# Optimization experiments

Measured on AMD Instinct MI355X. Metric: run time of the kernel, lower is better.

## Reference

```python
import jax, jax.numpy as jnp
import numpy as np

B, D_IN, D_FEAT, N_EX, N_LAB = 4096, 512, 512, 20000, 100
P_FACTOR = 3.0
EPS = 1e-12  # torch F.normalize eps


def setup_inputs() -> dict:
    key = jax.random.key(0)
    k1, k2, k3, k4 = jax.random.split(key, 4)
    features = jax.random.normal(k1, (B, D_IN), dtype=jnp.float32)
    g_weight = jax.random.normal(k2, (D_FEAT, D_IN), dtype=jnp.float32) * (1.0 / np.sqrt(D_IN))
    ex_features = jax.random.normal(k3, (N_EX, D_IN), dtype=jnp.float32)
    ex_classes = jax.random.uniform(k4, (N_EX, N_LAB), dtype=jnp.float32)
    class_reps = jnp.eye(N_LAB, dtype=jnp.float32)  # one_hot(arange(num_labels)) since class_dim is None
    return {"features": features, "g_weight": g_weight, "ex_features": ex_features,
            "ex_classes": ex_classes, "class_reps": class_reps}


def _l2_normalize(x):
    n = jnp.linalg.norm(x, axis=-1, keepdims=True)
    return x / jnp.maximum(n, EPS)


def _l1_normalize(x):
    n = jnp.sum(jnp.abs(x), axis=-1, keepdims=True)
    return x / jnp.maximum(n, EPS)


def reference(features, g_weight, ex_features, ex_classes, class_reps):
    # g projection (bias-free linear)
    f = features @ g_weight.T          # [B, D_FEAT]
    e = ex_features @ g_weight.T       # [N_EX, D_FEAT]
    # exemplar class representations
    ex_class_reps = _l1_normalize(ex_classes) @ class_reps  # [N_EX, N_LAB]
    # cosine similarity
    s = _l2_normalize(f) @ _l2_normalize(e).T  # [B, N_EX]
    # power-sign activation then L1 row-normalize
    a = jnp.sign(s) * jnp.abs(s) ** P_FACTOR
    a = _l1_normalize(a)
    echo = a @ ex_class_reps           # [B, N_LAB]
    return echo
```

## Files before the change

kernel.cpp:

```cpp
#include <hip/hip_runtime.h>

#define B_ROWS 4096
#define D      512
#define N_EX   20000
#define EXP2   20096
#define N_LAB  100
#define LABP2  128
#define NT2    157
#define SPLITS 16

typedef __attribute__((ext_vector_type(8)))  short short8v;
typedef __attribute__((ext_vector_type(4)))  short short4v;
typedef __attribute__((ext_vector_type(4)))  float f32x4;
typedef __attribute__((ext_vector_type(16))) float f32x16;
typedef __attribute__((ext_vector_type(2)))  int   int2v;
typedef unsigned short u16;

__device__ __forceinline__ u16 f2bf(float x) {
    unsigned u = __builtin_bit_cast(unsigned, x);
    u = u + 0x7FFFu + ((u >> 16) & 1u);
    return (u16)(u >> 16);
}
__device__ __forceinline__ float bf2f(u16 h) {
    unsigned u = ((unsigned)h) << 16;
    return __builtin_bit_cast(float, u);
}

__device__ __forceinline__ float wave_reduce_sum(float v) {
    #pragma unroll
    for (int off = 32; off > 0; off >>= 1) v += __shfl_down(v, off, 64);
    return v;
}

__device__ __forceinline__ void gload16(const void* g, void* l) {
    __builtin_amdgcn_global_load_lds((const __attribute__((address_space(1))) void*)g,
                                     (__attribute__((address_space(3))) void*)l, 16, 0, 0);
}

__device__ __forceinline__ unsigned pk_bf16(float a, float b) {
    unsigned r;
    asm("v_cvt_pk_bf16_f32 %0, %1, %2" : "=v"(r) : "v"(a), "v"(b));
    return r;
}

__device__ __forceinline__ void swap_halves(unsigned &a, unsigned &b) {
#if __has_builtin(__builtin_amdgcn_permlane32_swap)
    int2v r = __builtin_amdgcn_permlane32_swap((int)a, (int)b, false, false);
    a = (unsigned)r[0]; b = (unsigned)r[1];
#else
    unsigned sa = (unsigned)__shfl_xor((int)a, 32, 64);
    unsigned sb = (unsigned)__shfl_xor((int)b, 32, 64);
    if (threadIdx.x & 32) a = sb; else b = sa;
#endif
}

#define MFMA16(a, b, c) __builtin_amdgcn_mfma_f32_16x16x32_bf16((a), (b), (c), 0, 0, 0)
#define MFMA32(a, b, c) __builtin_amdgcn_mfma_f32_32x32x16_bf16((a), (b), (c), 0, 0, 0)

__global__ __launch_bounds__(256)
void splitH_k(const float* __restrict__ src, u16* __restrict__ dst,
              int src_rows, int dst_rows) {
    int i8 = blockIdx.x * 256 + threadIdx.x;
    if (i8 >= dst_rows * 64) return;
    int row = i8 >> 6;
    int e = (i8 & 63) * 8;
    short8v h = {0,0,0,0,0,0,0,0};
    if (row < src_rows) {
        const float* p = &src[(size_t)row * D + e];
        float4 a = *(const float4*)p, b = *(const float4*)(p + 4);
        float v[8] = {a.x,a.y,a.z,a.w,b.x,b.y,b.z,b.w};
        #pragma unroll
        for (int j = 0; j < 8; ++j) h[j] = (short)f2bf(v[j]);
    }
    *(short8v*)&dst[(size_t)row * D + e] = h;
}

__global__ __launch_bounds__(512, 4)
void gemm128_k(const u16* __restrict__ A, const u16* __restrict__ B,
               u16* __restrict__ C) {
    __shared__ u16 BUF[2][128][128];
    const int tid = threadIdx.x;
    const int l = tid & 63, w = tid >> 6;
    const int wa = w >> 2, wb = w & 3;
    const int l31 = l & 31, l5 = l >> 5;
    const int m0 = blockIdx.x * 128, n0 = blockIdx.y * 128;
    const int qrow_in = l >> 4;
    const int gs = l & 15;

    f32x16 sacc[2] = {};

    auto STAGE = [&](int nx, int kc_) {
        const int kofs = kc_ * 64;
        #pragma unroll
        for (int i = 0; i < 4; ++i) {
            const int q = w * 4 + i;
            const int r = q * 4 + qrow_in;
            const int g = gs ^ (r & 15);
            const u16* src = (g < 8)
                ? &A[(size_t)(m0 + r) * D + kofs + g * 8]
                : &B[(size_t)(n0 + r) * D + kofs + (g - 8) * 8];
            gload16(src, (u16*)&BUF[nx][0][0] + q * 512);
        }
    };

    STAGE(0, 0);
    __syncthreads();
    int cur = 0;
    for (int kc = 0; kc < 8; ++kc) {
        if (kc < 7) STAGE(cur ^ 1, kc + 1);
        const u16* base = &BUF[cur][0][0];
        #pragma unroll
        for (int ks = 0; ks < 4; ++ks) {
            const int gk = ks * 2 + l5;
            short8v aX[2], bW;
            #pragma unroll
            for (int ei = 0; ei < 2; ++ei) {
                int r = wa * 64 + ei * 32 + l31;
                aX[ei] = *(const short8v*)(base + r * 128 + (gk ^ (r & 15)) * 8);
            }
            {
                int r = wb * 32 + l31;
                bW = *(const short8v*)(base + r * 128 + ((gk | 8) ^ (r & 15)) * 8);
            }
            sacc[0] = MFMA32(aX[0], bW, sacc[0]);
            sacc[1] = MFMA32(aX[1], bW, sacc[1]);
        }
        __syncthreads();
        cur ^= 1;
    }
    #pragma unroll
    for (int ei = 0; ei < 2; ++ei)
        #pragma unroll
        for (int r = 0; r < 16; ++r) {
            int row = m0 + wa * 64 + ei * 32 + (r & 3) + 8 * (r >> 2) + 4 * l5;
            int col = n0 + wb * 32 + l31;
            C[(size_t)row * D + col] = f2bf(sacc[ei][r]);
        }
}

__global__ __launch_bounds__(256, 2)
void proj_k(const float* __restrict__ X, const float* __restrict__ W,
            u16* __restrict__ Chi, int M) {
    __shared__ u16 AH[64][72], AL[64][72], BH[64][72];
    const int tid = threadIdx.x;
    const int lane = tid & 63, wave = tid >> 6;
    const int wm = wave >> 1, wn = wave & 1;
    const int l15 = lane & 15, l4 = lane >> 4;
    const int m0 = blockIdx.x * 64, n0 = blockIdx.y * 64;
    f32x4 acc[2][2] = {};
    for (int kc = 0; kc < 8; ++kc) {
        __syncthreads();
        #pragma unroll
        for (int s = 0; s < 2; ++s) {
            int ix = tid + s * 256;
            int r = ix >> 3, c = ix & 7;
            float va[8] = {0.f,0.f,0.f,0.f,0.f,0.f,0.f,0.f};
            if (m0 + r < M) {
                const float* p = &X[(size_t)(m0 + r) * D + kc * 64 + c * 8];
                float4 t0 = *(const float4*)p, t1 = *(const float4*)(p + 4);
                va[0]=t0.x; va[1]=t0.y; va[2]=t0.z; va[3]=t0.w;
                va[4]=t1.x; va[5]=t1.y; va[6]=t1.z; va[7]=t1.w;
            }
            short8v h, l;
            #pragma unroll
            for (int j = 0; j < 8; ++j) {
                u16 hh = f2bf(va[j]); h[j] = (short)hh; l[j] = (short)f2bf(va[j] - bf2f(hh));
            }
            *(short8v*)&AH[r][c*8] = h; *(short8v*)&AL[r][c*8] = l;
            const float* q = &W[(size_t)(n0 + r) * D + kc * 64 + c * 8];
            float4 s0 = *(const float4*)q, s1 = *(const float4*)(q + 4);
            float vb[8] = {s0.x,s0.y,s0.z,s0.w,s1.x,s1.y,s1.z,s1.w};
            #pragma unroll
            for (int j = 0; j < 8; ++j) h[j] = (short)f2bf(vb[j]);
            *(short8v*)&BH[r][c*8] = h;
        }
        __syncthreads();
        #pragma unroll
        for (int ks = 0; ks < 2; ++ks) {
            const int ko = ks * 32 + l4 * 8;
            short8v ah0 = *(const short8v*)&AH[wm*32      + l15][ko];
            short8v ah1 = *(const short8v*)&AH[wm*32 + 16 + l15][ko];
            short8v al0 = *(const short8v*)&AL[wm*32      + l15][ko];
            short8v al1 = *(const short8v*)&AL[wm*32 + 16 + l15][ko];
            short8v bh0 = *(const short8v*)&BH[wn*32      + l15][ko];
            short8v bh1 = *(const short8v*)&BH[wn*32 + 16 + l15][ko];
            acc[0][0] = MFMA16(ah0, bh0, acc[0][0]); acc[0][0] = MFMA16(al0, bh0, acc[0][0]);
            acc[0][1] = MFMA16(ah0, bh1, acc[0][1]); acc[0][1] = MFMA16(al0, bh1, acc[0][1]);
            acc[1][0] = MFMA16(ah1, bh0, acc[1][0]); acc[1][0] = MFMA16(al1, bh0, acc[1][0]);
            acc[1][1] = MFMA16(ah1, bh1, acc[1][1]); acc[1][1] = MFMA16(al1, bh1, acc[1][1]);
        }
    }
    #pragma unroll
    for (int mi = 0; mi < 2; ++mi)
      #pragma unroll
      for (int ni = 0; ni < 2; ++ni)
        #pragma unroll
        for (int r = 0; r < 4; ++r) {
            int row = m0 + wm*32 + mi*16 + l4*4 + r;
            int col = n0 + wn*32 + ni*16 + l15;
            Chi[(size_t)row * D + col] = f2bf(acc[mi][ni][r]);
        }
}

__global__ __launch_bounds__(128)
void l2norm_k(u16* __restrict__ hi) {
    const int row = blockIdx.x, tid = threadIdx.x;
    const size_t base = (size_t)row * D + tid * 4;
    short4v hv = *(short4v*)&hi[base];
    float v[4]; float ss = 0.f;
    #pragma unroll
    for (int j = 0; j < 4; ++j) { v[j] = bf2f((u16)hv[j]); ss += v[j] * v[j]; }
    ss = wave_reduce_sum(ss);
    __shared__ float red[2];
    if ((tid & 63) == 0) red[tid >> 6] = ss;
    __syncthreads();
    float inv = 1.0f / fmaxf(sqrtf(red[0] + red[1]), 1e-12f);
    short4v ho;
    #pragma unroll
    for (int j = 0; j < 4; ++j) ho[j] = (short)f2bf(v[j] * inv);
    *(short4v*)&hi[base] = ho;
}

__global__ __launch_bounds__(256)
void ecrT_k(const float* __restrict__ exc, const float* __restrict__ creps,
            u16* __restrict__ th) {
    __shared__ float CRT[N_LAB][101];
    __shared__ float EX[128][N_LAB];
    __shared__ float INV[128];
    __shared__ u16 OUT[LABP2][128];
    const int tid = threadIdx.x;
    const int e0 = blockIdx.x * 128;
    for (int i = tid; i < N_LAB * N_LAB; i += 256) {
        int c = i / N_LAB, lab = i % N_LAB;
        CRT[lab][c] = creps[i];
    }
    for (int i = tid; i < 128 * N_LAB; i += 256) {
        int el = i / N_LAB, c = i % N_LAB;
        int e = e0 + el;
        EX[el][c] = (e < N_EX) ? exc[(size_t)e * N_LAB + c] : 0.f;
    }
    __syncthreads();
    if (tid < 128) {
        float s = 0.f;
        for (int c = 0; c < N_LAB; ++c) s += fabsf(EX[tid][c]);
        INV[tid] = 1.0f / fmaxf(s, 1e-12f);
    }
    __syncthreads();
    const int lab = tid & 127;
    for (int el = tid >> 7; el < 128; el += 2) {
        float acc = 0.f;
        if (lab < N_LAB) {
            #pragma unroll 4
            for (int c = 0; c < N_LAB; ++c) acc += EX[el][c] * CRT[lab][c];
            acc *= INV[el];
        }
        OUT[lab][el] = f2bf(acc);
    }
    __syncthreads();
    for (int i = tid; i < LABP2 * 16; i += 256) {
        int lb = i >> 4, ch = i & 15;
        *(short8v*)&th[(size_t)lb * EXP2 + e0 + ch * 8] = *(const short8v*)&OUT[lb][ch * 8];
    }
}

__global__ __launch_bounds__(512, 4)
void fused_k(const u16* __restrict__ fnh, const u16* __restrict__ enh,
             const u16* __restrict__ ecth,
             float* __restrict__ nump, float* __restrict__ denp2) {
    __shared__ u16 BUF[2][128][128];
    const int tid = threadIdx.x;
    const int l = tid & 63, w = tid >> 6;
    const int we = w >> 2, wq = w & 3;
    const int l31 = l & 31, l5 = l >> 5;
    const int m0 = blockIdx.x * 128;
    const int split = blockIdx.y;
    const int qrow_in = l >> 4;
    const int gs = l & 15;

    union FragU { short8v s; unsigned u[4]; };

    f32x16 num_acc[4] = {};
    float den_th = 0.f;

    auto STAGE_AB = [&](int nx, int t_, int kc_) {
        const int e0_ = t_ * 128, kofs = kc_ * 64;
        #pragma unroll
        for (int i = 0; i < 4; ++i) {
            const int q = w * 4 + i;
            const int r = q * 4 + qrow_in;
            const int g = gs ^ (r & 15);
            const u16* src = (g < 8)
                ? &enh[(size_t)(e0_ + r) * D + kofs + g * 8]
                : &fnh[(size_t)(m0 + r) * D + kofs + (g - 8) * 8];
            gload16(src, (u16*)&BUF[nx][0][0] + q * 512);
        }
    };
    auto STAGE_WT = [&](int nx, int t_) {
        const int e0_ = t_ * 128;
        #pragma unroll
        for (int i = 0; i < 4; ++i) {
            const int q = w * 4 + i;
            const int lab = q * 4 + qrow_in;
            const int g = gs ^ (lab & 15);
            gload16(&ecth[(size_t)lab * EXP2 + e0_ + g * 8],
                    (u16*)&BUF[nx][0][0] + q * 512);
        }
    };

    STAGE_AB(0, split, 0);
    __syncthreads();
    int cur = 0;

    for (int t = split; t < NT2; t += SPLITS) {
        f32x16 sacc[2] = {};
        for (int kc = 0; kc < 8; ++kc) {
            if (kc < 7) STAGE_AB(cur ^ 1, t, kc + 1);
            else        STAGE_WT(cur ^ 1, t);
            const u16* base = &BUF[cur][0][0];
            #pragma unroll
            for (int ks = 0; ks < 4; ++ks) {
                const int gk = ks * 2 + l5;
                short8v aE[2], bF;
                #pragma unroll
                for (int ei = 0; ei < 2; ++ei) {
                    int r = we * 64 + ei * 32 + l31;
                    aE[ei] = *(const short8v*)(base + r * 128 + (gk ^ (r & 15)) * 8);
                }
                {
                    int r = wq * 32 + l31;
                    bF = *(const short8v*)(base + r * 128 + ((gk | 8) ^ (r & 15)) * 8);
                }
                sacc[0] = MFMA32(aE[0], bF, sacc[0]);
                sacc[1] = MFMA32(aE[1], bF, sacc[1]);
            }
            __syncthreads();
            cur ^= 1;
        }
        const int tn = t + SPLITS;
        if (tn < NT2) STAGE_AB(cur ^ 1, tn, 0);
        const u16* wbase = &BUF[cur][0][0];
        #pragma unroll
        for (int ei = 0; ei < 2; ++ei) {
            float a3[16];
            #pragma unroll
            for (int r = 0; r < 16; ++r) {
                float sv = sacc[ei][r];
                float c3 = sv * sv * sv;
                a3[r] = c3;
                den_th += fabsf(c3);
            }
            FragU fr[2];
            #pragma unroll
            for (int c = 0; c < 2; ++c) {
                unsigned p01 = pk_bf16(a3[c*8+0], a3[c*8+1]);
                unsigned p23 = pk_bf16(a3[c*8+2], a3[c*8+3]);
                unsigned p45 = pk_bf16(a3[c*8+4], a3[c*8+5]);
                unsigned p67 = pk_bf16(a3[c*8+6], a3[c*8+7]);
                swap_halves(p01, p45);
                swap_halves(p23, p67);
                fr[c].u[0] = p01; fr[c].u[1] = p23; fr[c].u[2] = p45; fr[c].u[3] = p67;
            }
            #pragma unroll
            for (int c = 0; c < 2; ++c) {
                const int gw = (we * 4 + ei * 2 + c) * 2 + l5;
                #pragma unroll
                for (int lt = 0; lt < 4; ++lt) {
                    int row = lt * 32 + l31;
                    short8v wf = *(const short8v*)(wbase + row * 128 + (gw ^ (row & 15)) * 8);
                    num_acc[lt] = MFMA32(fr[c].s, wf, num_acc[lt]);
                }
            }
        }
        __syncthreads();
        cur ^= 1;
    }

    {
        float v = den_th;
        v += __shfl_xor(v, 32, 64);
        if (l5 == 0)
            denp2[((size_t)split * 2 + we) * B_ROWS + m0 + wq * 32 + l31] = v;
    }

    float* SMf = (float*)&BUF[0][0][0];
    __syncthreads();
    #pragma unroll
    for (int half = 0; half < 2; ++half) {
        if (we == 1 && (wq >> 1) == half) {
            #pragma unroll
            for (int lt = 0; lt < 4; ++lt)
                #pragma unroll
                for (int r = 0; r < 16; ++r) {
                    int rowf = (r & 3) + 8 * (r >> 2) + 4 * l5;
                    SMf[((wq & 1) * 32 + rowf) * 128 + lt * 32 + l31] = num_acc[lt][r];
                }
        }
        __syncthreads();
        if (we == 0 && (wq >> 1) == half) {
            #pragma unroll
            for (int lt = 0; lt < 4; ++lt)
                #pragma unroll
                for (int r = 0; r < 16; ++r) {
                    int rowf = (r & 3) + 8 * (r >> 2) + 4 * l5;
                    float v = num_acc[lt][r] + SMf[((wq & 1) * 32 + rowf) * 128 + lt * 32 + l31];
                    int m = m0 + wq * 32 + rowf;
                    nump[((size_t)split * B_ROWS + m) * LABP2 + lt * 32 + l31] = v;
                }
        }
        __syncthreads();
    }
}

__global__ __launch_bounds__(128)
void finalize_k(const float* __restrict__ nump, const float* __restrict__ denp2,
                float* __restrict__ out) {
    const int row = blockIdx.x, tid = threadIdx.x;
    float den = 0.f;
    for (int s = 0; s < 2 * SPLITS; ++s)
        den += denp2[(size_t)s * B_ROWS + row];
    if (tid < N_LAB) {
        float acc = 0.f;
        for (int s = 0; s < SPLITS; ++s)
            acc += nump[((size_t)s * B_ROWS + row) * LABP2 + tid];
        out[(size_t)row * N_LAB + tid] = acc / fmaxf(den, 1e-12f);
    }
}

extern "C" void kernel_launch(void* const* d_in, const int* in_sizes, int n_in,
                              void* d_out, int out_size, void* d_ws, size_t ws_size,
                              hipStream_t stream) {
    (void)in_sizes; (void)n_in; (void)out_size; (void)ws_size;
    const float* features    = (const float*)d_in[0];
    const float* g_weight    = (const float*)d_in[1];
    const float* ex_features = (const float*)d_in[2];
    const float* ex_classes  = (const float*)d_in[3];
    const float* class_reps  = (const float*)d_in[4];
    float* out = (float*)d_out;

    size_t off = 0;
    auto alloc = [&](size_t bytes) {
        void* p = (char*)d_ws + off;
        off += (bytes + 255) & ~(size_t)255;
        return p;
    };
    u16* fnh = (u16*)alloc((size_t)B_ROWS * D * 2);
    u16* enh = (u16*)alloc((size_t)EXP2 * D * 2);
    u16* ecth = (u16*)alloc((size_t)LABP2 * EXP2 * 2);
    u16* wh  = (u16*)alloc((size_t)D * D * 2);
    float* nump  = (float*)alloc((size_t)SPLITS * B_ROWS * LABP2 * 4);
    float* denp2 = (float*)alloc((size_t)2 * SPLITS * B_ROWS * 4);
    u16* exh = (u16*)nump;

    splitH_k<<<(EXP2 * 64 + 255) / 256, 256, 0, stream>>>(ex_features, exh, N_EX, EXP2);
    splitH_k<<<(D * 64 + 255) / 256, 256, 0, stream>>>(g_weight, wh, D, D);
    gemm128_k<<<dim3(EXP2 / 128, 4), 512, 0, stream>>>(exh, wh, enh);
    proj_k<<<dim3(B_ROWS / 64, 8), 256, 0, stream>>>(features, g_weight, fnh, B_ROWS);
    l2norm_k<<<B_ROWS, 128, 0, stream>>>(fnh);
    l2norm_k<<<EXP2, 128, 0, stream>>>(enh);
    ecrT_k<<<NT2, 256, 0, stream>>>(ex_classes, class_reps, ecth);
    fused_k<<<dim3(B_ROWS / 128, SPLITS), 512, 0, stream>>>(fnh, enh, ecth, nump, denp2);
    finalize_k<<<B_ROWS, 128, 0, stream>>>(nump, denp2, out);
}
```

Baseline: 432.1 us.

## Merge feature/exemplar projections into one GEMM and widen fused tile to 256 rows

Features and exemplars are now converted to bf16 into one contiguous buffer and projected by a single gemm128_k launch, followed by one l2norm launch. This replaces the separate hi/lo-split proj_k kernel and the second l2norm launch, so the feature projection no longer carries the low-order correction term. fused_k now processes 256 query rows per block instead of 128, using separate LDS regions for exemplar, feature and class-weight tiles. Each exemplar tile and class-weight fragment is therefore reused across twice as many rows. In exchange the block needs 128 KB of LDS, the grid halves to 256 blocks, occupancy drops, and register pressure rises.

```diff
diff --git a/kernel.cpp b/kernel.cpp
--- a/kernel.cpp
+++ b/kernel.cpp
@@ -4,6 +4,7 @@
 #define D      512
 #define N_EX   20000
 #define EXP2   20096
+#define MPROJ  24192
 #define N_LAB  100
 #define LABP2  128
 #define NT2    157
@@ -11,7 +12,6 @@
 
 typedef __attribute__((ext_vector_type(8)))  short short8v;
 typedef __attribute__((ext_vector_type(4)))  short short4v;
-typedef __attribute__((ext_vector_type(4)))  float f32x4;
 typedef __attribute__((ext_vector_type(16))) float f32x16;
 typedef __attribute__((ext_vector_type(2)))  int   int2v;
 typedef unsigned short u16;
@@ -54,7 +54,6 @@
 #endif
 }
 
-#define MFMA16(a, b, c) __builtin_amdgcn_mfma_f32_16x16x32_bf16((a), (b), (c), 0, 0, 0)
 #define MFMA32(a, b, c) __builtin_amdgcn_mfma_f32_32x32x16_bf16((a), (b), (c), 0, 0, 0)
 
 __global__ __launch_bounds__(256)
@@ -138,70 +137,6 @@
         }
 }
 
-__global__ __launch_bounds__(256, 2)
-void proj_k(const float* __restrict__ X, const float* __restrict__ W,
-            u16* __restrict__ Chi, int M) {
-    __shared__ u16 AH[64][72], AL[64][72], BH[64][72];
-    const int tid = threadIdx.x;
-    const int lane = tid & 63, wave = tid >> 6;
-    const int wm = wave >> 1, wn = wave & 1;
-    const int l15 = lane & 15, l4 = lane >> 4;
-    const int m0 = blockIdx.x * 64, n0 = blockIdx.y * 64;
-    f32x4 acc[2][2] = {};
-    for (int kc = 0; kc < 8; ++kc) {
-        __syncthreads();
-        #pragma unroll
-        for (int s = 0; s < 2; ++s) {
-            int ix = tid + s * 256;
-            int r = ix >> 3, c = ix & 7;
-            float va[8] = {0.f,0.f,0.f,0.f,0.f,0.f,0.f,0.f};
-            if (m0 + r < M) {
-                const float* p = &X[(size_t)(m0 + r) * D + kc * 64 + c * 8];
-                float4 t0 = *(const float4*)p, t1 = *(const float4*)(p + 4);
-                va[0]=t0.x; va[1]=t0.y; va[2]=t0.z; va[3]=t0.w;
-                va[4]=t1.x; va[5]=t1.y; va[6]=t1.z; va[7]=t1.w;
-            }
-            short8v h, l;
-            #pragma unroll
-            for (int j = 0; j < 8; ++j) {
-                u16 hh = f2bf(va[j]); h[j] = (short)hh; l[j] = (short)f2bf(va[j] - bf2f(hh));
-            }
-            *(short8v*)&AH[r][c*8] = h; *(short8v*)&AL[r][c*8] = l;
-            const float* q = &W[(size_t)(n0 + r) * D + kc * 64 + c * 8];
-            float4 s0 = *(const float4*)q, s1 = *(const float4*)(q + 4);
-            float vb[8] = {s0.x,s0.y,s0.z,s0.w,s1.x,s1.y,s1.z,s1.w};
-            #pragma unroll
-            for (int j = 0; j < 8; ++j) h[j] = (short)f2bf(vb[j]);
-            *(short8v*)&BH[r][c*8] = h;
-        }
-        __syncthreads();
-        #pragma unroll
-        for (int ks = 0; ks < 2; ++ks) {
-            const int ko = ks * 32 + l4 * 8;
-            short8v ah0 = *(const short8v*)&AH[wm*32      + l15][ko];
-            short8v ah1 = *(const short8v*)&AH[wm*32 + 16 + l15][ko];
-            short8v al0 = *(const short8v*)&AL[wm*32      + l15][ko];
-            short8v al1 = *(const short8v*)&AL[wm*32 + 16 + l15][ko];
-            short8v bh0 = *(const short8v*)&BH[wn*32      + l15][ko];
-            short8v bh1 = *(const short8v*)&BH[wn*32 + 16 + l15][ko];
-            acc[0][0] = MFMA16(ah0, bh0, acc[0][0]); acc[0][0] = MFMA16(al0, bh0, acc[0][0]);
-            acc[0][1] = MFMA16(ah0, bh1, acc[0][1]); acc[0][1] = MFMA16(al0, bh1, acc[0][1]);
-            acc[1][0] = MFMA16(ah1, bh0, acc[1][0]); acc[1][0] = MFMA16(al1, bh0, acc[1][0]);
-            acc[1][1] = MFMA16(ah1, bh1, acc[1][1]); acc[1][1] = MFMA16(al1, bh1, acc[1][1]);
-        }
-    }
-    #pragma unroll
-    for (int mi = 0; mi < 2; ++mi)
-      #pragma unroll
-      for (int ni = 0; ni < 2; ++ni)
-        #pragma unroll
-        for (int r = 0; r < 4; ++r) {
-            int row = m0 + wm*32 + mi*16 + l4*4 + r;
-            int col = n0 + wn*32 + ni*16 + l15;
-            Chi[(size_t)row * D + col] = f2bf(acc[mi][ni][r]);
-        }
-}
-
 __global__ __launch_bounds__(128)
 void l2norm_k(u16* __restrict__ hi) {
     const int row = blockIdx.x, tid = threadIdx.x;
@@ -263,47 +198,52 @@
     }
 }
 
-__global__ __launch_bounds__(512, 4)
+__global__ __launch_bounds__(512, 2)
 void fused_k(const u16* __restrict__ fnh, const u16* __restrict__ enh,
              const u16* __restrict__ ecth,
              float* __restrict__ nump, float* __restrict__ denp2) {
-    __shared__ u16 BUF[2][128][128];
+    __shared__ u16 SMEM[65536];
+    u16* ENR = SMEM;
+    u16* FNR = SMEM + 16384;
+    u16* WTB = SMEM + 49152;
+
     const int tid = threadIdx.x;
     const int l = tid & 63, w = tid >> 6;
     const int we = w >> 2, wq = w & 3;
     const int l31 = l & 31, l5 = l >> 5;
-    const int m0 = blockIdx.x * 128;
+    const int m0 = blockIdx.x * 256;
     const int split = blockIdx.y;
-    const int qrow_in = l >> 4;
-    const int gs = l & 15;
 
     union FragU { short8v s; unsigned u[4]; };
 
-    f32x16 num_acc[4] = {};
-    float den_th = 0.f;
+    f32x16 num_acc[2][4] = {};
+    float den_th[2] = {0.f, 0.f};
 
     auto STAGE_AB = [&](int nx, int t_, int kc_) {
         const int e0_ = t_ * 128, kofs = kc_ * 64;
         #pragma unroll
+        for (int i = 0; i < 2; ++i) {
+            const int ge = w * 128 + i * 64 + l;
+            const int row = ge >> 3, g = ge & 7;
+            gload16(&enh[(size_t)(e0_ + row) * D + kofs + ((g ^ (row & 7)) * 8)],
+                    ENR + nx * 8192 + (w * 128 + i * 64) * 8);
+        }
+        #pragma unroll
         for (int i = 0; i < 4; ++i) {
-            const int q = w * 4 + i;
-            const int r = q * 4 + qrow_in;
-            const int g = gs ^ (r & 15);
-            const u16* src = (g < 8)
-                ? &enh[(size_t)(e0_ + r) * D + kofs + g * 8]
-                : &fnh[(size_t)(m0 + r) * D + kofs + (g - 8) * 8];
-            gload16(src, (u16*)&BUF[nx][0][0] + q * 512);
+            const int gf = w * 256 + i * 64 + l;
+            const int row = gf >> 3, g = gf & 7;
+            gload16(&fnh[(size_t)(m0 + row) * D + kofs + ((g ^ (row & 7)) * 8)],
+                    FNR + nx * 16384 + (w * 256 + i * 64) * 8);
         }
     };
-    auto STAGE_WT = [&](int nx, int t_) {
+    auto STAGE_WT = [&](int t_) {
         const int e0_ = t_ * 128;
         #pragma unroll
         for (int i = 0; i < 4; ++i) {
-            const int q = w * 4 + i;
-            const int lab = q * 4 + qrow_in;
-            const int g = gs ^ (lab & 15);
-            gload16(&ecth[(size_t)lab * EXP2 + e0_ + g * 8],
-                    (u16*)&BUF[nx][0][0] + q * 512);
+            const int gwt = w * 256 + i * 64 + l;
+            const int lab = gwt >> 4, g = gwt & 15;
+            gload16(&ecth[(size_t)lab * EXP2 + e0_ + ((g ^ (lab & 15)) * 8)],
+                    WTB + (w * 256 + i * 64) * 8);
         }
     };
 
@@ -312,53 +252,61 @@
     int cur = 0;
 
     for (int t = split; t < NT2; t += SPLITS) {
-        f32x16 sacc[2] = {};
+        f32x16 sacc[2][2] = {};
         for (int kc = 0; kc < 8; ++kc) {
             if (kc < 7) STAGE_AB(cur ^ 1, t, kc + 1);
-            else        STAGE_WT(cur ^ 1, t);
-            const u16* base = &BUF[cur][0][0];
+            else        STAGE_WT(t);
+            const u16* eb = ENR + cur * 8192;
+            const u16* fb = FNR + cur * 16384;
             #pragma unroll
             for (int ks = 0; ks < 4; ++ks) {
                 const int gk = ks * 2 + l5;
-                short8v aE[2], bF;
+                short8v aE[2], bF[2];
                 #pragma unroll
                 for (int ei = 0; ei < 2; ++ei) {
                     int r = we * 64 + ei * 32 + l31;
-                    aE[ei] = *(const short8v*)(base + r * 128 + (gk ^ (r & 15)) * 8);
+                    aE[ei] = *(const short8v*)(eb + r * 64 + (gk ^ (r & 7)) * 8);
                 }
-                {
-                    int r = wq * 32 + l31;
-                    bF = *(const short8v*)(base + r * 128 + ((gk | 8) ^ (r & 15)) * 8);
+                #pragma unroll
+                for (int mi = 0; mi < 2; ++mi) {
+                    int r = wq * 64 + mi * 32 + l31;
+                    bF[mi] = *(const short8v*)(fb + r * 64 + (gk ^ (r & 7)) * 8);
                 }
-                sacc[0] = MFMA32(aE[0], bF, sacc[0]);
-                sacc[1] = MFMA32(aE[1], bF, sacc[1]);
+                #pragma unroll
+                for (int ei = 0; ei < 2; ++ei)
+                    #pragma unroll
+                    for (int mi = 0; mi < 2; ++mi)
+                        sacc[ei][mi] = MFMA32(aE[ei], bF[mi], sacc[ei][mi]);
             }
             __syncthreads();
-            cur ^= 1;
+            if (kc < 7) cur ^= 1;
         }
         const int tn = t + SPLITS;
         if (tn < NT2) STAGE_AB(cur ^ 1, tn, 0);
-        const u16* wbase = &BUF[cur][0][0];
         #pragma unroll
         for (int ei = 0; ei < 2; ++ei) {
-            float a3[16];
-            #pragma unroll
-            for (int r = 0; r < 16; ++r) {
-                float sv = sacc[ei][r];
-                float c3 = sv * sv * sv;
-                a3[r] = c3;
-                den_th += fabsf(c3);
-            }
-            FragU fr[2];
-            #pragma unroll
-            for (int c = 0; c < 2; ++c) {
-                unsigned p01 = pk_bf16(a3[c*8+0], a3[c*8+1]);
-                unsigned p23 = pk_bf16(a3[c*8+2], a3[c*8+3]);
-                unsigned p45 = pk_bf16(a3[c*8+4], a3[c*8+5]);
-                unsigned p67 = pk_bf16(a3[c*8+6], a3[c*8+7]);
-                swap_halves(p01, p45);
-                swap_halves(p23, p67);
-                fr[c].u[0] = p01; fr[c].u[1] = p23; fr[c].u[2] = p45; fr[c].u[3] = p67;
+            FragU fr[2][2];
+            #pragma unroll
+            for (int mi = 0; mi < 2; ++mi) {
+                float a3[16];
+                #pragma unroll
+                for (int r = 0; r < 16; ++r) {
+                    float sv = sacc[ei][mi][r];
+                    float c3 = sv * sv * sv;
+                    a3[r] = c3;
+                    den_th[mi] += fabsf(c3);
+                }
+                #pragma unroll
+                for (int c = 0; c < 2; ++c) {
+                    unsigned p01 = pk_bf16(a3[c*8+0], a3[c*8+1]);
+                    unsigned p23 = pk_bf16(a3[c*8+2], a3[c*8+3]);
+                    unsigned p45 = pk_bf16(a3[c*8+4], a3[c*8+5]);
+                    unsigned p67 = pk_bf16(a3[c*8+6], a3[c*8+7]);
+                    swap_halves(p01, p45);
+                    swap_halves(p23, p67);
+                    fr[mi][c].u[0] = p01; fr[mi][c].u[1] = p23;
+                    fr[mi][c].u[2] = p45; fr[mi][c].u[3] = p67;
+                }
             }
             #pragma unroll
             for (int c = 0; c < 2; ++c) {
@@ -366,8 +314,9 @@
                 #pragma unroll
                 for (int lt = 0; lt < 4; ++lt) {
                     int row = lt * 32 + l31;
-                    short8v wf = *(const short8v*)(wbase + row * 128 + (gw ^ (row & 15)) * 8);
-                    num_acc[lt] = MFMA32(fr[c].s, wf, num_acc[lt]);
+                    short8v wf = *(const short8v*)(WTB + row * 128 + (gw ^ (row & 15)) * 8);
+                    num_acc[0][lt] = MFMA32(fr[0][c].s, wf, num_acc[0][lt]);
+                    num_acc[1][lt] = MFMA32(fr[1][c].s, wf, num_acc[1][lt]);
                 }
             }
         }
@@ -375,37 +324,44 @@
         cur ^= 1;
     }
 
-    {
-        float v = den_th;
+    #pragma unroll
+    for (int mi = 0; mi < 2; ++mi) {
+        float v = den_th[mi];
         v += __shfl_xor(v, 32, 64);
         if (l5 == 0)
-            denp2[((size_t)split * 2 + we) * B_ROWS + m0 + wq * 32 + l31] = v;
-    }
-
-    float* SMf = (float*)&BUF[0][0][0];
+            denp2[((size_t)split * 2 + we) * B_ROWS + m0 + wq * 64 + mi * 32 + l31] = v;
+    }
+
+    float* SMf = (float*)SMEM;
     __syncthreads();
     #pragma unroll
     for (int half = 0; half < 2; ++half) {
         if (we == 1 && (wq >> 1) == half) {
             #pragma unroll
-            for (int lt = 0; lt < 4; ++lt)
-                #pragma unroll
-                for (int r = 0; r < 16; ++r) {
-                    int rowf = (r & 3) + 8 * (r >> 2) + 4 * l5;
-                    SMf[((wq & 1) * 32 + rowf) * 128 + lt * 32 + l31] = num_acc[lt][r];
-                }
+            for (int mi = 0; mi < 2; ++mi)
+                #pragma unroll
+                for (int lt = 0; lt < 4; ++lt)
+                    #pragma unroll
+                    for (int r = 0; r < 16; ++r) {
+                        int rowf = (r & 3) + 8 * (r >> 2) + 4 * l5;
+                        int lrow = (wq & 1) * 64 + mi * 32 + rowf;
+                        SMf[lrow * 128 + lt * 32 + l31] = num_acc[mi][lt][r];
+                    }
         }
         __syncthreads();
         if (we == 0 && (wq >> 1) == half) {
             #pragma unroll
-            for (int lt = 0; lt < 4; ++lt)
-                #pragma unroll
-                for (int r = 0; r < 16; ++r) {
-                    int rowf = (r & 3) + 8 * (r >> 2) + 4 * l5;
-                    float v = num_acc[lt][r] + SMf[((wq & 1) * 32 + rowf) * 128 + lt * 32 + l31];
-                    int m = m0 + wq * 32 + rowf;
-                    nump[((size_t)split * B_ROWS + m) * LABP2 + lt * 32 + l31] = v;
-                }
+            for (int mi = 0; mi < 2; ++mi)
+                #pragma unroll
+                for (int lt = 0; lt < 4; ++lt)
+                    #pragma unroll
+                    for (int r = 0; r < 16; ++r) {
+                        int rowf = (r & 3) + 8 * (r >> 2) + 4 * l5;
+                        int lrow = (wq & 1) * 64 + mi * 32 + rowf;
+                        float v = num_acc[mi][lt][r] + SMf[lrow * 128 + lt * 32 + l31];
+                        int m = m0 + wq * 64 + mi * 32 + rowf;
+                        nump[((size_t)split * B_ROWS + m) * LABP2 + lt * 32 + l31] = v;
+                    }
         }
         __syncthreads();
     }
@@ -449,15 +405,14 @@
     u16* wh  = (u16*)alloc((size_t)D * D * 2);
     float* nump  = (float*)alloc((size_t)SPLITS * B_ROWS * LABP2 * 4);
     float* denp2 = (float*)alloc((size_t)2 * SPLITS * B_ROWS * 4);
-    u16* exh = (u16*)nump;
-
-    splitH_k<<<(EXP2 * 64 + 255) / 256, 256, 0, stream>>>(ex_features, exh, N_EX, EXP2);
+    u16* xall = (u16*)nump;
+
+    splitH_k<<<(B_ROWS * 64 + 255) / 256, 256, 0, stream>>>(features, xall, B_ROWS, B_ROWS);
+    splitH_k<<<(EXP2 * 64 + 255) / 256, 256, 0, stream>>>(ex_features, xall + (size_t)B_ROWS * D, N_EX, EXP2);
     splitH_k<<<(D * 64 + 255) / 256, 256, 0, stream>>>(g_weight, wh, D, D);
-    gemm128_k<<<dim3(EXP2 / 128, 4), 512, 0, stream>>>(exh, wh, enh);
-    proj_k<<<dim3(B_ROWS / 64, 8), 256, 0, stream>>>(features, g_weight, fnh, B_ROWS);
-    l2norm_k<<<B_ROWS, 128, 0, stream>>>(fnh);
-    l2norm_k<<<EXP2, 128, 0, stream>>>(enh);
+    gemm128_k<<<dim3(MPROJ / 128, 4), 512, 0, stream>>>(xall, wh, fnh);
+    l2norm_k<<<MPROJ, 128, 0, stream>>>(fnh);
     ecrT_k<<<NT2, 256, 0, stream>>>(ex_classes, class_reps, ecth);
-    fused_k<<<dim3(B_ROWS / 128, SPLITS), 512, 0, stream>>>(fnh, enh, ecth, nump, denp2);
+    fused_k<<<dim3(B_ROWS / 256, SPLITS), 512, 0, stream>>>(fnh, enh, ecth, nump, denp2);
     finalize_k<<<B_ROWS, 128, 0, stream>>>(nump, denp2, out);
 }
```

New measurement: 380.7 us. 11.9% less time.
